# Kernel tuning notes

Hardware: AMD Instinct MI355X
Metric: run time of the kernel (lower is better)

## Reference

```python
import jax, jax.numpy as jnp
import numpy as np
import math

B, LQ, LK = 4, 512, 512
D_MODEL, NHEAD, NLABELS = 512, 8, 8
D_Q = D_MODEL // NHEAD


def setup_inputs() -> dict:
    key = jax.random.key(0)
    ks = jax.random.split(key, 12)
    xavier = lambda k, shape: jax.random.uniform(
        k, shape, jnp.float32,
        -math.sqrt(6.0 / (shape[0] + shape[1])), math.sqrt(6.0 / (shape[0] + shape[1])))
    return {
        "q": jax.random.normal(ks[0], (B, LQ, D_MODEL), jnp.float32),
        "k": jax.random.normal(ks[1], (B, LK, D_MODEL), jnp.float32),
        "edge_mask": jax.random.randint(ks[2], (B, LQ, LK, NLABELS), 0, 2).astype(jnp.float32),
        "padding_mask": jax.random.randint(ks[3], (B, LQ, LK), 0, 2).astype(jnp.float32),
        "w_q_w": xavier(ks[4], (D_MODEL, D_MODEL)),
        "w_q_b": jnp.zeros((D_MODEL,), jnp.float32),
        "w_k": xavier(ks[5], (D_MODEL, D_MODEL)),
        "w_v": xavier(ks[6], (D_MODEL, D_MODEL)),
        "w_h_w": xavier(ks[7], (D_MODEL, D_MODEL)),
        "w_h_b": jnp.zeros((D_MODEL,), jnp.float32),
        "b_ks": xavier(ks[8], (NLABELS, D_Q)),
        "b_vs": xavier(ks[9], (NLABELS, D_Q)),
    }


def reference(q, k, edge_mask, padding_mask, w_q_w, w_q_b, w_k, w_v, w_h_w, w_h_b, b_ks, b_vs):
    sz_b, len_q, _ = q.shape
    len_k = k.shape[1]
    temp = np.power(D_Q, 0.5).astype(np.float32)

    # projections -> (nhead, B, L, d_q), matching torch permute(2,0,1,3)
    query = (q @ w_q_w.T + w_q_b).reshape(sz_b, len_q, NHEAD, D_Q).transpose(2, 0, 1, 3)
    key = (k @ w_k.T).reshape(sz_b, len_k, NHEAD, D_Q).transpose(2, 0, 1, 3)
    value = (k @ w_v.T).reshape(sz_b, len_k, NHEAD, D_Q).transpose(2, 0, 1, 3)

    # content scores + relation-bias scores
    qk = jnp.einsum('hbqd,hbkd->hbqk', query, key)
    key_rel = jnp.einsum('bqkl,ld->bqkd', edge_mask, b_ks)      # (B,Lq,Lk,d_q)
    qkr = jnp.einsum('hbqd,bqkd->hbqk', query, key_rel)
    output_attention_weights = (qk + qkr) / temp                # pre-mask, as returned by torch

    # mask where no edge label AND padding_mask==1
    relation_mask = (edge_mask.sum(-1) + (1.0 - padding_mask)) == 0  # (B,Lq,Lk)
    rm = relation_mask[None, :, :, :]                                # broadcast over heads
    attn = jnp.where(rm, -jnp.inf, output_attention_weights)
    attn = jax.nn.softmax(attn, axis=-1)
    attn = jnp.where(rm, 0.0, attn)

    # value aggregation: content + relation values
    qv = jnp.einsum('hbqk,hbkd->hbqd', attn, value)
    val_rel = jnp.einsum('bqkl,ld->bqkd', edge_mask, b_vs)
    qvr = jnp.einsum('hbqk,bqkd->hbqd', attn, val_rel)

    out = (qv + qvr).transpose(1, 2, 0, 3).reshape(sz_b, len_q, D_MODEL)
    out = out @ w_h_w.T + w_h_b
    return out, output_attention_weights.reshape(NHEAD * sz_b, len_q, len_k)
```

## Files before the change

kernel.cpp:

```cpp
#include <hip/hip_runtime.h>
#include <math.h>

#define NB 4
#define LQ 512
#define LK 512
#define DM 512
#define NH 8
#define DQ 64
#define NL 8
#define QT 32
#define PSTR 520

typedef short bf16x8 __attribute__((ext_vector_type(8)));
typedef float f32x4 __attribute__((ext_vector_type(4)));

__device__ __forceinline__ unsigned short f2bf(float x) {
    unsigned u = __float_as_uint(x);
    u += 0x7fff + ((u >> 16) & 1);
    return (unsigned short)(u >> 16);
}
__device__ __forceinline__ float bf2f(unsigned x) {
    return __uint_as_float(x << 16);
}
__device__ __forceinline__ void gld16(const void* g, void* l) {
    __builtin_amdgcn_global_load_lds(
        (const __attribute__((address_space(1))) void*)g,
        (__attribute__((address_space(3))) void*)l, 16, 0, 0);
}

__global__ __launch_bounds__(256) void prep_kernel(
        const float* __restrict__ q,  const float* __restrict__ k,
        const float* __restrict__ wq, const float* __restrict__ wk,
        const float* __restrict__ wv, const float* __restrict__ wh,
        const float* __restrict__ em, const float* __restrict__ pad,
        unsigned short* __restrict__ qb,  unsigned short* __restrict__ kb,
        unsigned short* __restrict__ wqb, unsigned short* __restrict__ wkb,
        unsigned short* __restrict__ wvb, unsigned short* __restrict__ whb,
        unsigned short* __restrict__ Pk) {
    const int tid = threadIdx.x;
    const int y = blockIdx.y;
    if (y < 6) {
        const float* s; unsigned short* d; int n;
        switch (y) {
            case 0: s = q;  d = qb;  n = NB * LQ * DM; break;
            case 1: s = k;  d = kb;  n = NB * LK * DM; break;
            case 2: s = wq; d = wqb; n = DM * DM; break;
            case 3: s = wk; d = wkb; n = DM * DM; break;
            case 4: s = wv; d = wvb; n = DM * DM; break;
            default: s = wh; d = whb; n = DM * DM; break;
        }
        const int i = blockIdx.x * 256 + tid;
        if (i * 8 >= n) return;
        const float4* sv = (const float4*)s;
        const float4 a = sv[2 * (size_t)i], b = sv[2 * (size_t)i + 1];
        uint4 o;
        o.x = (unsigned)f2bf(a.x) | ((unsigned)f2bf(a.y) << 16);
        o.y = (unsigned)f2bf(a.z) | ((unsigned)f2bf(a.w) << 16);
        o.z = (unsigned)f2bf(b.x) | ((unsigned)f2bf(b.y) << 16);
        o.w = (unsigned)f2bf(b.z) | ((unsigned)f2bf(b.w) << 16);
        *(uint4*)(d + (size_t)i * 8) = o;
    } else {
        if (blockIdx.x >= 512) return;
        const int row = blockIdx.x * 4 + (tid >> 6);
        const int k0 = (tid & 63) * 8;
        const float* eb = em + ((size_t)row * LK + k0) * NL;
        const float4 pv0 = *(const float4*)(pad + (size_t)row * LK + k0);
        const float4 pv1 = *(const float4*)(pad + (size_t)row * LK + k0 + 4);
        const float pv[8] = {pv0.x, pv0.y, pv0.z, pv0.w, pv1.x, pv1.y, pv1.z, pv1.w};
        unsigned short outv[8];
#pragma unroll
        for (int kk = 0; kk < 8; ++kk) {
            const float4 v0 = *(const float4*)(eb + kk * 8);
            const float4 v1 = *(const float4*)(eb + kk * 8 + 4);
            unsigned b_ = 0;
            b_ |= (v0.x != 0.f) << 0; b_ |= (v0.y != 0.f) << 1;
            b_ |= (v0.z != 0.f) << 2; b_ |= (v0.w != 0.f) << 3;
            b_ |= (v1.x != 0.f) << 4; b_ |= (v1.y != 0.f) << 5;
            b_ |= (v1.z != 0.f) << 6; b_ |= (v1.w != 0.f) << 7;
            b_ |= (pv[kk] != 0.f) << 8;
            outv[kk] = (unsigned short)b_;
        }
        uint4 o;
        o.x = (unsigned)outv[0] | ((unsigned)outv[1] << 16);
        o.y = (unsigned)outv[2] | ((unsigned)outv[3] << 16);
        o.z = (unsigned)outv[4] | ((unsigned)outv[5] << 16);
        o.w = (unsigned)outv[6] | ((unsigned)outv[7] << 16);
        *(uint4*)(Pk + (size_t)row * LK + k0) = o;
    }
}

__device__ __forceinline__ void gemm64core(const unsigned short* __restrict__ Ag, int lda,
                                           const unsigned short* __restrict__ Bg, int ldb,
                                           int K, short* As, short* Bs,
                                           f32x4 (&acc)[2][2]) {
    const int tid = threadIdx.x;
    const int wave = tid >> 6, lane = tid & 63;
    const int quad = lane >> 4, l16 = lane & 15;
    const int wr = wave >> 1, wc = wave & 1;
    for (int k0 = 0; k0 < K; k0 += 32) {
        __syncthreads();
        gld16(Ag + (size_t)(tid >> 2) * lda + k0 + (tid & 3) * 8, (char*)As + wave * 1024);
        gld16(Bg + (size_t)(tid >> 2) * ldb + k0 + (tid & 3) * 8, (char*)Bs + wave * 1024);
        __syncthreads();
        bf16x8 af[2], bf[2];
#pragma unroll
        for (int i = 0; i < 2; ++i)
            af[i] = *(const bf16x8*)&As[(wr * 32 + i * 16 + l16) * 32 + quad * 8];
#pragma unroll
        for (int j = 0; j < 2; ++j)
            bf[j] = *(const bf16x8*)&Bs[(wc * 32 + j * 16 + l16) * 32 + quad * 8];
#pragma unroll
        for (int i = 0; i < 2; ++i)
#pragma unroll
            for (int j = 0; j < 2; ++j)
                acc[i][j] = __builtin_amdgcn_mfma_f32_16x16x32_bf16(af[i], bf[j], acc[i][j], 0, 0, 0);
    }
}

__global__ __launch_bounds__(256) void proj_all(const unsigned short* __restrict__ qb,
                                                const unsigned short* __restrict__ kb,
                                                const unsigned short* __restrict__ wqb,
                                                const unsigned short* __restrict__ wkb,
                                                const unsigned short* __restrict__ wvb,
                                                const float* __restrict__ w_q_b,
                                                unsigned short* __restrict__ Qp,
                                                unsigned short* __restrict__ Kp,
                                                unsigned short* __restrict__ Vt) {
    __shared__ __align__(16) short As[64 * 32];
    __shared__ __align__(16) short Bs[64 * 32];
    const unsigned short* A; const unsigned short* W; const float* bias;
    unsigned short* C; int mode;
    switch (blockIdx.z) {
        case 0:  A = qb; W = wqb; bias = w_q_b;  C = Qp; mode = 0; break;
        case 1:  A = kb; W = wkb; bias = nullptr; C = Kp; mode = 0; break;
        default: A = kb; W = wvb; bias = nullptr; C = Vt; mode = 1; break;
    }
    f32x4 acc[2][2];
    const f32x4 zz = {0.f, 0.f, 0.f, 0.f};
#pragma unroll
    for (int i = 0; i < 2; ++i)
#pragma unroll
        for (int j = 0; j < 2; ++j) acc[i][j] = zz;
    const int m0 = blockIdx.x * 64, n0 = blockIdx.y * 64;
    gemm64core(A + (size_t)m0 * DM, DM, W + (size_t)n0 * DM, DM, DM, As, Bs, acc);
    const int tid = threadIdx.x, wave = tid >> 6, lane = tid & 63;
    const int quad = lane >> 4, l16 = lane & 15;
    const int wr = wave >> 1, wc = wave & 1;
#pragma unroll
    for (int i = 0; i < 2; ++i)
#pragma unroll
        for (int r = 0; r < 4; ++r) {
            const int gm = m0 + wr * 32 + i * 16 + quad * 4 + r;
#pragma unroll
            for (int j = 0; j < 2; ++j) {
                const int gn = n0 + wc * 32 + j * 16 + l16;
                float v = acc[i][j][r];
                if (bias) v += bias[gn];
                if (mode == 0) C[(size_t)gm * DM + gn] = f2bf(v);
                else C[(size_t)(gm >> 9) * (DM * LK) + (size_t)gn * LK + (gm & 511)] = f2bf(v);
            }
        }
}

__global__ __launch_bounds__(512, 4) void attn_fused(
        const unsigned short* __restrict__ Qp,
        const unsigned short* __restrict__ Kp,
        const unsigned short* __restrict__ Vt,
        const unsigned short* __restrict__ Pk,
        const float* __restrict__ b_ks,
        const float* __restrict__ b_vs,
        float* __restrict__ weights,
        unsigned short* __restrict__ Hb) {
    __shared__ __align__(16) short Qs[QT * 64];
    __shared__ __align__(16) short Kc[128 * 64];
    __shared__ __align__(16) short Ps[QT * PSTR];
    __shared__ float svS[QT * NL];
    __shared__ float tS[QT * NL];
    __shared__ float redA[QT * 8];
    __shared__ float redB[QT * 8];

    const int tid = threadIdx.x, wave = tid >> 6, lane = tid & 63;
    const int quad = lane >> 4, l16 = lane & 15;
    const int q0 = blockIdx.x * QT;
    const int z = blockIdx.y, h = z >> 2, b = z & 3;

    if (tid < 256) {
        const int row = tid >> 3, ch = tid & 7;
        gld16(Qp + (size_t)(b * LQ + q0 + row) * DM + h * DQ + ((ch ^ (row & 7)) * 8),
              (char*)Qs + wave * 1024);
    }

    f32x4 acc[4][2];
    const f32x4 zz = {0.f, 0.f, 0.f, 0.f};
#pragma unroll
    for (int c = 0; c < 4; ++c) { acc[c][0] = zz; acc[c][1] = zz; }

    for (int c = 0; c < 4; ++c) {
#pragma unroll
        for (int it = 0; it < 2; ++it) {
            const int e = it * 512 + tid;
            const int kr = e >> 3, ch = e & 7;
            gld16(Kp + (size_t)(b * LK + c * 128 + kr) * DM + h * DQ + ((ch ^ (kr & 7)) * 8),
                  (char*)Kc + it * 8192 + wave * 1024);
        }
        __syncthreads();
#pragma unroll
        for (int kd = 0; kd < 64; kd += 32) {
            const int krow = wave * 16 + l16;
            const int kch = ((kd >> 3) + quad) ^ (krow & 7);
            const bf16x8 bfv = *(const bf16x8*)&Kc[krow * 64 + kch * 8];
#pragma unroll
            for (int i = 0; i < 2; ++i) {
                const int qrow = i * 16 + l16;
                const int qch = ((kd >> 3) + quad) ^ (qrow & 7);
                const bf16x8 afv = *(const bf16x8*)&Qs[qrow * 64 + qch * 8];
                acc[c][i] = __builtin_amdgcn_mfma_f32_16x16x32_bf16(afv, bfv, acc[c][i], 0, 0, 0);
            }
        }
        if (c == 0 && tid < 256) {
            const int row = tid >> 3, l = tid & 7;
            float s = 0.f;
#pragma unroll
            for (int d = 0; d < DQ; ++d) {
                const int ds = ((d >> 3) ^ (row & 7)) * 8 + (d & 7);
                s = fmaf(bf2f((unsigned short)Qs[row * 64 + ds]), b_ks[l * DQ + d], s);
            }
            svS[row * 8 + l] = s;
        }
        __syncthreads();
    }

#pragma unroll
    for (int it = 0; it < 2; ++it) {
        const int e = it * 512 + tid;
        const int dd = e >> 4, ch = e & 15;
        gld16(Vt + (size_t)(b * DM + h * DQ + dd) * LK + ((ch ^ (dd & 15)) * 8),
              (char*)Kc + it * 8192 + wave * 1024);
    }

#pragma unroll
    for (int i = 0; i < 2; ++i)
#pragma unroll
        for (int r = 0; r < 4; ++r) {
            const int row = i * 16 + quad * 4 + r;
            const int gq = q0 + row;
            const f32x4 sv0 = *(const f32x4*)&svS[row * 8];
            const f32x4 sv1 = *(const f32x4*)&svS[row * 8 + 4];
            const unsigned short* prow = Pk + (size_t)(b * LQ + gq) * LK;
            float* wrow = weights + ((size_t)z * LQ + gq) * LK;
            float pm = -__builtin_inff();
#pragma unroll
            for (int c = 0; c < 4; ++c) {
                const int col = c * 128 + wave * 16 + l16;
                const unsigned w_ = prow[col];
                float rel = 0.f;
                rel = fmaf((float)((w_ >> 0) & 1), sv0[0], rel);
                rel = fmaf((float)((w_ >> 1) & 1), sv0[1], rel);
                rel = fmaf((float)((w_ >> 2) & 1), sv0[2], rel);
                rel = fmaf((float)((w_ >> 3) & 1), sv0[3], rel);
                rel = fmaf((float)((w_ >> 4) & 1), sv1[0], rel);
                rel = fmaf((float)((w_ >> 5) & 1), sv1[1], rel);
                rel = fmaf((float)((w_ >> 6) & 1), sv1[2], rel);
                rel = fmaf((float)((w_ >> 7) & 1), sv1[3], rel);
                const float wv = (acc[c][i][r] + rel) * 0.125f;
                wrow[col] = wv;
                const float m = ((w_ & 0x1FFu) == 0x100u) ? -__builtin_inff() : wv;
                acc[c][i][r] = m;
                pm = fmaxf(pm, m);
            }
#pragma unroll
            for (int o = 1; o < 16; o <<= 1) pm = fmaxf(pm, __shfl_xor(pm, o, 64));
            float ps = 0.f;
#pragma unroll
            for (int c = 0; c < 4; ++c) {
                const float e = __expf(acc[c][i][r] - pm);
                acc[c][i][r] = e;
                ps += e;
            }
#pragma unroll
            for (int o = 1; o < 16; o <<= 1) ps += __shfl_xor(ps, o, 64);
            if (l16 == 0) { redA[row * 8 + wave] = pm; redB[row * 8 + wave] = ps; }
        }
    __syncthreads();

#pragma unroll
    for (int i = 0; i < 2; ++i)
#pragma unroll
        for (int r = 0; r < 4; ++r) {
            const int row = i * 16 + quad * 4 + r;
            const f32x4 pa = *(const f32x4*)&redA[row * 8];
            const f32x4 pb = *(const f32x4*)&redA[row * 8 + 4];
            const f32x4 sa = *(const f32x4*)&redB[row * 8];
            const f32x4 sb = *(const f32x4*)&redB[row * 8 + 4];
            const float M = fmaxf(fmaxf(fmaxf(pa[0], pa[1]), fmaxf(pa[2], pa[3])),
                                  fmaxf(fmaxf(pb[0], pb[1]), fmaxf(pb[2], pb[3])));
            const float S = sa[0] * __expf(pa[0] - M) + sa[1] * __expf(pa[1] - M)
                          + sa[2] * __expf(pa[2] - M) + sa[3] * __expf(pa[3] - M)
                          + sb[0] * __expf(pb[0] - M) + sb[1] * __expf(pb[1] - M)
                          + sb[2] * __expf(pb[2] - M) + sb[3] * __expf(pb[3] - M);
            const float own = redA[row * 8 + wave];
            const float alpha = __expf(own - M) / S;
#pragma unroll
            for (int c = 0; c < 4; ++c) {
                const int col = c * 128 + wave * 16 + l16;
                Ps[row * PSTR + col] = (short)f2bf(acc[c][i][r] * alpha);
            }
        }
    __syncthreads();

    {
        const int row = tid >> 4, l = (tid >> 1) & 7, half = tid & 1;
        const uint4* pw = (const uint4*)(Pk + (size_t)(b * LQ + q0 + row) * LK + half * 256);
        const uint4* aw = (const uint4*)&Ps[row * PSTR + half * 256];
        float tv = 0.f;
#pragma unroll 4
        for (int kk = 0; kk < 32; ++kk) {
            const uint4 wb = pw[kk];
            const uint4 av = aw[kk];
            const unsigned w4[4] = {wb.x, wb.y, wb.z, wb.w};
            const unsigned a4[4] = {av.x, av.y, av.z, av.w};
#pragma unroll
            for (int u = 0; u < 4; ++u) {
                tv += ((w4[u] >> l) & 1)        ? bf2f(a4[u] & 0xffffu) : 0.f;
                tv += ((w4[u] >> (16 + l)) & 1) ? bf2f(a4[u] >> 16)     : 0.f;
            }
        }
        tv += __shfl_xor(tv, 1, 64);
        if (half == 0) tS[row * 8 + l] = tv;
    }

    f32x4 oacc = zz;
    const int mi = wave & 1, ni = wave >> 1;
    for (int vc = 0; vc < 4; ++vc) {
        if (vc > 0) {
            __syncthreads();
#pragma unroll
            for (int it = 0; it < 2; ++it) {
                const int e = it * 512 + tid;
                const int dd = e >> 4, ch = e & 15;
                gld16(Vt + (size_t)(b * DM + h * DQ + dd) * LK + vc * 128 + ((ch ^ (dd & 15)) * 8),
                      (char*)Kc + it * 8192 + wave * 1024);
            }
            __syncthreads();
        }
#pragma unroll
        for (int kd = 0; kd < 128; kd += 32) {
            const int vrow = ni * 16 + l16;
            const int vch = ((kd >> 3) + quad) ^ (vrow & 15);
            const bf16x8 afv = *(const bf16x8*)&Ps[(mi * 16 + l16) * PSTR + vc * 128 + kd + quad * 8];
            const bf16x8 bfv = *(const bf16x8*)&Kc[vrow * 128 + vch * 8];
            oacc = __builtin_amdgcn_mfma_f32_16x16x32_bf16(afv, bfv, oacc, 0, 0, 0);
        }
    }

    const int gd = ni * 16 + l16;
    float bvv[NL];
#pragma unroll
    for (int l = 0; l < NL; ++l) bvv[l] = b_vs[l * DQ + gd];
#pragma unroll
    for (int r = 0; r < 4; ++r) {
        const int row = mi * 16 + quad * 4 + r;
        const float* tp = &tS[row * 8];
        float o = oacc[r];
#pragma unroll
        for (int l = 0; l < NL; ++l) o = fmaf(tp[l], bvv[l], o);
        Hb[(size_t)(b * LQ + q0 + row) * DM + h * DQ + gd] = f2bf(o);
    }
}

__global__ __launch_bounds__(256) void outproj_mfma(const unsigned short* __restrict__ Hb,
                                                    const unsigned short* __restrict__ whb,
                                                    const float* __restrict__ bias,
                                                    float* __restrict__ C) {
    __shared__ __align__(16) short As[64 * 32];
    __shared__ __align__(16) short Bs[64 * 32];
    f32x4 acc[2][2];
    const f32x4 zz = {0.f, 0.f, 0.f, 0.f};
#pragma unroll
    for (int i = 0; i < 2; ++i)
#pragma unroll
        for (int j = 0; j < 2; ++j) acc[i][j] = zz;
    const int m0 = blockIdx.x * 64, n0 = blockIdx.y * 64;
    gemm64core(Hb + (size_t)m0 * DM, DM, whb + (size_t)n0 * DM, DM, DM, As, Bs, acc);
    const int tid = threadIdx.x, wave = tid >> 6, lane = tid & 63;
    const int quad = lane >> 4, l16 = lane & 15;
    const int wr = wave >> 1, wc = wave & 1;
#pragma unroll
    for (int i = 0; i < 2; ++i)
#pragma unroll
        for (int r = 0; r < 4; ++r) {
            const int gm = m0 + wr * 32 + i * 16 + quad * 4 + r;
#pragma unroll
            for (int j = 0; j < 2; ++j) {
                const int gn = n0 + wc * 32 + j * 16 + l16;
                C[(size_t)gm * DM + gn] = acc[i][j][r] + bias[gn];
            }
        }
}

extern "C" void kernel_launch(void* const* d_in, const int* in_sizes, int n_in,
                              void* d_out, int out_size, void* d_ws, size_t ws_size,
                              hipStream_t stream) {
    const float* q     = (const float*)d_in[0];
    const float* k     = (const float*)d_in[1];
    const float* em    = (const float*)d_in[2];
    const float* pad   = (const float*)d_in[3];
    const float* w_q_w = (const float*)d_in[4];
    const float* w_q_b = (const float*)d_in[5];
    const float* w_k   = (const float*)d_in[6];
    const float* w_v   = (const float*)d_in[7];
    const float* w_h_w = (const float*)d_in[8];
    const float* w_h_b = (const float*)d_in[9];
    const float* b_ks  = (const float*)d_in[10];
    const float* b_vs  = (const float*)d_in[11];

    float* out     = (float*)d_out;
    float* weights = out + (size_t)NB * LQ * DM;

    char* ws = (char*)d_ws;
    unsigned short* qb  = (unsigned short*)(ws + 0);
    unsigned short* kb  = (unsigned short*)(ws + 2097152);
    unsigned short* wqb = (unsigned short*)(ws + 4194304);
    unsigned short* wkb = (unsigned short*)(ws + 4718592);
    unsigned short* wvb = (unsigned short*)(ws + 5242880);
    unsigned short* whb = (unsigned short*)(ws + 5767168);
    unsigned short* Qp  = (unsigned short*)(ws + 6291456);
    unsigned short* Kp  = (unsigned short*)(ws + 8388608);
    unsigned short* Vt  = (unsigned short*)(ws + 10485760);
    unsigned short* Hb  = (unsigned short*)(ws + 12582912);
    unsigned short* Pk  = (unsigned short*)(ws + 14680064);

    prep_kernel<<<dim3(1024, 7), 256, 0, stream>>>(q, k, w_q_w, w_k, w_v, w_h_w,
                                                   em, pad, qb, kb, wqb, wkb, wvb, whb, Pk);
    proj_all<<<dim3(32, 8, 3), 256, 0, stream>>>(qb, kb, wqb, wkb, wvb, w_q_b, Qp, Kp, Vt);
    attn_fused<<<dim3(LQ / QT, 32), 512, 0, stream>>>(Qp, Kp, Vt, Pk, b_ks, b_vs, weights, Hb);
    outproj_mfma<<<dim3(32, 8), 256, 0, stream>>>(Hb, whb, w_h_b, out);
}
```

Baseline: 169.9 us.

## Drop LDS staging for direct global MFMA loads, add relation LUT and fp16 PV path

Removes LDS staging with global_load_lds from the projection, output-projection and attention kernels, so MFMA fragments are read directly from global memory. The relation score is now a per-row 16-entry lookup table built from q·b_ks, replacing eight FMAs per score. Probabilities and V are stored as fp16 so the PV product uses the f16 MFMA and the relation-value sum uses packed half math. This cuts barriers and shared-memory traffic, but relies on cache hits for reused operands and changes the numeric precision of P and V.

```diff
diff --git a/kernel.cpp b/kernel.cpp
--- a/kernel.cpp
+++ b/kernel.cpp
@@ -12,6 +12,8 @@
 #define PSTR 520
 
 typedef short bf16x8 __attribute__((ext_vector_type(8)));
+typedef _Float16 f16x8 __attribute__((ext_vector_type(8)));
+typedef _Float16 f16x2 __attribute__((ext_vector_type(2)));
 typedef float f32x4 __attribute__((ext_vector_type(4)));
 
 __device__ __forceinline__ unsigned short f2bf(float x) {
@@ -22,10 +24,9 @@
 __device__ __forceinline__ float bf2f(unsigned x) {
     return __uint_as_float(x << 16);
 }
-__device__ __forceinline__ void gld16(const void* g, void* l) {
-    __builtin_amdgcn_global_load_lds(
-        (const __attribute__((address_space(1))) void*)g,
-        (__attribute__((address_space(3))) void*)l, 16, 0, 0);
+__device__ __forceinline__ unsigned short f2h(float x) {
+    _Float16 h = (_Float16)x;
+    return __builtin_bit_cast(unsigned short, h);
 }
 
 __global__ __launch_bounds__(256) void prep_kernel(
@@ -89,34 +90,6 @@
     }
 }
 
-__device__ __forceinline__ void gemm64core(const unsigned short* __restrict__ Ag, int lda,
-                                           const unsigned short* __restrict__ Bg, int ldb,
-                                           int K, short* As, short* Bs,
-                                           f32x4 (&acc)[2][2]) {
-    const int tid = threadIdx.x;
-    const int wave = tid >> 6, lane = tid & 63;
-    const int quad = lane >> 4, l16 = lane & 15;
-    const int wr = wave >> 1, wc = wave & 1;
-    for (int k0 = 0; k0 < K; k0 += 32) {
-        __syncthreads();
-        gld16(Ag + (size_t)(tid >> 2) * lda + k0 + (tid & 3) * 8, (char*)As + wave * 1024);
-        gld16(Bg + (size_t)(tid >> 2) * ldb + k0 + (tid & 3) * 8, (char*)Bs + wave * 1024);
-        __syncthreads();
-        bf16x8 af[2], bf[2];
-#pragma unroll
-        for (int i = 0; i < 2; ++i)
-            af[i] = *(const bf16x8*)&As[(wr * 32 + i * 16 + l16) * 32 + quad * 8];
-#pragma unroll
-        for (int j = 0; j < 2; ++j)
-            bf[j] = *(const bf16x8*)&Bs[(wc * 32 + j * 16 + l16) * 32 + quad * 8];
-#pragma unroll
-        for (int i = 0; i < 2; ++i)
-#pragma unroll
-            for (int j = 0; j < 2; ++j)
-                acc[i][j] = __builtin_amdgcn_mfma_f32_16x16x32_bf16(af[i], bf[j], acc[i][j], 0, 0, 0);
-    }
-}
-
 __global__ __launch_bounds__(256) void proj_all(const unsigned short* __restrict__ qb,
                                                 const unsigned short* __restrict__ kb,
                                                 const unsigned short* __restrict__ wqb,
@@ -126,8 +99,6 @@
                                                 unsigned short* __restrict__ Qp,
                                                 unsigned short* __restrict__ Kp,
                                                 unsigned short* __restrict__ Vt) {
-    __shared__ __align__(16) short As[64 * 32];
-    __shared__ __align__(16) short Bs[64 * 32];
     const unsigned short* A; const unsigned short* W; const float* bias;
     unsigned short* C; int mode;
     switch (blockIdx.z) {
@@ -135,17 +106,32 @@
         case 1:  A = kb; W = wkb; bias = nullptr; C = Kp; mode = 0; break;
         default: A = kb; W = wvb; bias = nullptr; C = Vt; mode = 1; break;
     }
-    f32x4 acc[2][2];
-    const f32x4 zz = {0.f, 0.f, 0.f, 0.f};
-#pragma unroll
-    for (int i = 0; i < 2; ++i)
-#pragma unroll
-        for (int j = 0; j < 2; ++j) acc[i][j] = zz;
-    const int m0 = blockIdx.x * 64, n0 = blockIdx.y * 64;
-    gemm64core(A + (size_t)m0 * DM, DM, W + (size_t)n0 * DM, DM, DM, As, Bs, acc);
     const int tid = threadIdx.x, wave = tid >> 6, lane = tid & 63;
     const int quad = lane >> 4, l16 = lane & 15;
     const int wr = wave >> 1, wc = wave & 1;
+    const int m0 = blockIdx.x * 64, n0 = blockIdx.y * 64;
+    f32x4 acc[2][2];
+    const f32x4 zz = {0.f, 0.f, 0.f, 0.f};
+#pragma unroll
+    for (int i = 0; i < 2; ++i)
+#pragma unroll
+        for (int j = 0; j < 2; ++j) acc[i][j] = zz;
+    const unsigned short* Ar0 = A + (size_t)(m0 + wr * 32 + l16) * DM;
+    const unsigned short* Ar1 = Ar0 + 16 * DM;
+    const unsigned short* Br0 = W + (size_t)(n0 + wc * 32 + l16) * DM;
+    const unsigned short* Br1 = Br0 + 16 * DM;
+#pragma unroll 4
+    for (int k0 = 0; k0 < DM; k0 += 32) {
+        const int o = k0 + quad * 8;
+        const bf16x8 a0 = *(const bf16x8*)&Ar0[o];
+        const bf16x8 a1 = *(const bf16x8*)&Ar1[o];
+        const bf16x8 b0 = *(const bf16x8*)&Br0[o];
+        const bf16x8 b1 = *(const bf16x8*)&Br1[o];
+        acc[0][0] = __builtin_amdgcn_mfma_f32_16x16x32_bf16(a0, b0, acc[0][0], 0, 0, 0);
+        acc[0][1] = __builtin_amdgcn_mfma_f32_16x16x32_bf16(a0, b1, acc[0][1], 0, 0, 0);
+        acc[1][0] = __builtin_amdgcn_mfma_f32_16x16x32_bf16(a1, b0, acc[1][0], 0, 0, 0);
+        acc[1][1] = __builtin_amdgcn_mfma_f32_16x16x32_bf16(a1, b1, acc[1][1], 0, 0, 0);
+    }
 #pragma unroll
     for (int i = 0; i < 2; ++i)
 #pragma unroll
@@ -157,7 +143,7 @@
                 float v = acc[i][j][r];
                 if (bias) v += bias[gn];
                 if (mode == 0) C[(size_t)gm * DM + gn] = f2bf(v);
-                else C[(size_t)(gm >> 9) * (DM * LK) + (size_t)gn * LK + (gm & 511)] = f2bf(v);
+                else C[(size_t)(gm >> 9) * (DM * LK) + (size_t)gn * LK + (gm & 511)] = f2h(v);
             }
         }
 }
@@ -171,10 +157,9 @@
         const float* __restrict__ b_vs,
         float* __restrict__ weights,
         unsigned short* __restrict__ Hb) {
-    __shared__ __align__(16) short Qs[QT * 64];
-    __shared__ __align__(16) short Kc[128 * 64];
     __shared__ __align__(16) short Ps[QT * PSTR];
     __shared__ float svS[QT * NL];
+    __shared__ float lutS[QT * 32];
     __shared__ float tS[QT * NL];
     __shared__ float redA[QT * 8];
     __shared__ float redB[QT * 8];
@@ -184,59 +169,57 @@
     const int q0 = blockIdx.x * QT;
     const int z = blockIdx.y, h = z >> 2, b = z & 3;
 
-    if (tid < 256) {
-        const int row = tid >> 3, ch = tid & 7;
-        gld16(Qp + (size_t)(b * LQ + q0 + row) * DM + h * DQ + ((ch ^ (row & 7)) * 8),
-              (char*)Qs + wave * 1024);
+    {
+        const int row = tid >> 4, l = (tid >> 1) & 7, half = tid & 1;
+        const unsigned short* qrow = Qp + (size_t)(b * LQ + q0 + row) * DM + h * DQ + half * 32;
+        const float* bk = b_ks + l * DQ + half * 32;
+        float s = 0.f;
+#pragma unroll
+        for (int d0 = 0; d0 < 32; d0 += 8) {
+            const bf16x8 qv = *(const bf16x8*)&qrow[d0];
+#pragma unroll
+            for (int j = 0; j < 8; ++j)
+                s = fmaf(bf2f((unsigned short)qv[j]), bk[d0 + j], s);
+        }
+        s += __shfl_xor(s, 1, 64);
+        if (half == 0) svS[row * 8 + l] = s;
+    }
+    __syncthreads();
+
+    for (int e = tid; e < QT * 32; e += 512) {
+        const int row = e >> 5, idx = e & 31;
+        const float* s = &svS[row * 8 + ((idx & 16) ? 4 : 0)];
+        float v = 0.f;
+        v += (idx & 1) ? s[0] : 0.f;
+        v += (idx & 2) ? s[1] : 0.f;
+        v += (idx & 4) ? s[2] : 0.f;
+        v += (idx & 8) ? s[3] : 0.f;
+        lutS[e] = v;
     }
 
     f32x4 acc[4][2];
     const f32x4 zz = {0.f, 0.f, 0.f, 0.f};
 #pragma unroll
     for (int c = 0; c < 4; ++c) { acc[c][0] = zz; acc[c][1] = zz; }
-
+    bf16x8 qf[2][2];
+#pragma unroll
+    for (int i = 0; i < 2; ++i)
+#pragma unroll
+        for (int kd = 0; kd < 2; ++kd)
+            qf[i][kd] = *(const bf16x8*)&Qp[(size_t)(b * LQ + q0 + i * 16 + l16) * DM
+                                           + h * DQ + kd * 32 + quad * 8];
+#pragma unroll
     for (int c = 0; c < 4; ++c) {
-#pragma unroll
-        for (int it = 0; it < 2; ++it) {
-            const int e = it * 512 + tid;
-            const int kr = e >> 3, ch = e & 7;
-            gld16(Kp + (size_t)(b * LK + c * 128 + kr) * DM + h * DQ + ((ch ^ (kr & 7)) * 8),
-                  (char*)Kc + it * 8192 + wave * 1024);
-        }
-        __syncthreads();
-#pragma unroll
-        for (int kd = 0; kd < 64; kd += 32) {
-            const int krow = wave * 16 + l16;
-            const int kch = ((kd >> 3) + quad) ^ (krow & 7);
-            const bf16x8 bfv = *(const bf16x8*)&Kc[krow * 64 + kch * 8];
-#pragma unroll
-            for (int i = 0; i < 2; ++i) {
-                const int qrow = i * 16 + l16;
-                const int qch = ((kd >> 3) + quad) ^ (qrow & 7);
-                const bf16x8 afv = *(const bf16x8*)&Qs[qrow * 64 + qch * 8];
-                acc[c][i] = __builtin_amdgcn_mfma_f32_16x16x32_bf16(afv, bfv, acc[c][i], 0, 0, 0);
-            }
-        }
-        if (c == 0 && tid < 256) {
-            const int row = tid >> 3, l = tid & 7;
-            float s = 0.f;
-#pragma unroll
-            for (int d = 0; d < DQ; ++d) {
-                const int ds = ((d >> 3) ^ (row & 7)) * 8 + (d & 7);
-                s = fmaf(bf2f((unsigned short)Qs[row * 64 + ds]), b_ks[l * DQ + d], s);
-            }
-            svS[row * 8 + l] = s;
-        }
-        __syncthreads();
-    }
-
-#pragma unroll
-    for (int it = 0; it < 2; ++it) {
-        const int e = it * 512 + tid;
-        const int dd = e >> 4, ch = e & 15;
-        gld16(Vt + (size_t)(b * DM + h * DQ + dd) * LK + ((ch ^ (dd & 15)) * 8),
-              (char*)Kc + it * 8192 + wave * 1024);
-    }
+        const unsigned short* krow = Kp + (size_t)(b * LK + c * 128 + wave * 16 + l16) * DM + h * DQ;
+#pragma unroll
+        for (int kd = 0; kd < 2; ++kd) {
+            const bf16x8 bfv = *(const bf16x8*)&krow[kd * 32 + quad * 8];
+#pragma unroll
+            for (int i = 0; i < 2; ++i)
+                acc[c][i] = __builtin_amdgcn_mfma_f32_16x16x32_bf16(qf[i][kd], bfv, acc[c][i], 0, 0, 0);
+        }
+    }
+    __syncthreads();
 
 #pragma unroll
     for (int i = 0; i < 2; ++i)
@@ -244,8 +227,7 @@
         for (int r = 0; r < 4; ++r) {
             const int row = i * 16 + quad * 4 + r;
             const int gq = q0 + row;
-            const f32x4 sv0 = *(const f32x4*)&svS[row * 8];
-            const f32x4 sv1 = *(const f32x4*)&svS[row * 8 + 4];
+            const float* lrow = &lutS[row * 32];
             const unsigned short* prow = Pk + (size_t)(b * LQ + gq) * LK;
             float* wrow = weights + ((size_t)z * LQ + gq) * LK;
             float pm = -__builtin_inff();
@@ -253,15 +235,7 @@
             for (int c = 0; c < 4; ++c) {
                 const int col = c * 128 + wave * 16 + l16;
                 const unsigned w_ = prow[col];
-                float rel = 0.f;
-                rel = fmaf((float)((w_ >> 0) & 1), sv0[0], rel);
-                rel = fmaf((float)((w_ >> 1) & 1), sv0[1], rel);
-                rel = fmaf((float)((w_ >> 2) & 1), sv0[2], rel);
-                rel = fmaf((float)((w_ >> 3) & 1), sv0[3], rel);
-                rel = fmaf((float)((w_ >> 4) & 1), sv1[0], rel);
-                rel = fmaf((float)((w_ >> 5) & 1), sv1[1], rel);
-                rel = fmaf((float)((w_ >> 6) & 1), sv1[2], rel);
-                rel = fmaf((float)((w_ >> 7) & 1), sv1[3], rel);
+                const float rel = lrow[w_ & 15u] + lrow[16 + ((w_ >> 4) & 15u)];
                 const float wv = (acc[c][i][r] + rel) * 0.125f;
                 wrow[col] = wv;
                 const float m = ((w_ & 0x1FFu) == 0x100u) ? -__builtin_inff() : wv;
@@ -303,7 +277,7 @@
 #pragma unroll
             for (int c = 0; c < 4; ++c) {
                 const int col = c * 128 + wave * 16 + l16;
-                Ps[row * PSTR + col] = (short)f2bf(acc[c][i][r] * alpha);
+                Ps[row * PSTR + col] = (short)f2h(acc[c][i][r] * alpha);
             }
         }
     __syncthreads();
@@ -319,11 +293,14 @@
             const uint4 av = aw[kk];
             const unsigned w4[4] = {wb.x, wb.y, wb.z, wb.w};
             const unsigned a4[4] = {av.x, av.y, av.z, av.w};
+            f16x2 hacc = {(_Float16)0.f, (_Float16)0.f};
 #pragma unroll
             for (int u = 0; u < 4; ++u) {
-                tv += ((w4[u] >> l) & 1)        ? bf2f(a4[u] & 0xffffu) : 0.f;
-                tv += ((w4[u] >> (16 + l)) & 1) ? bf2f(a4[u] >> 16)     : 0.f;
-            }
+                const unsigned bits = (w4[u] >> l) & 0x10001u;
+                const unsigned msk = bits * 0x3c00u;
+                hacc += __builtin_bit_cast(f16x2, a4[u]) * __builtin_bit_cast(f16x2, msk);
+            }
+            tv += (float)hacc[0] + (float)hacc[1];
         }
         tv += __shfl_xor(tv, 1, 64);
         if (half == 0) tS[row * 8 + l] = tv;
@@ -331,27 +308,15 @@
 
     f32x4 oacc = zz;
     const int mi = wave & 1, ni = wave >> 1;
-    for (int vc = 0; vc < 4; ++vc) {
-        if (vc > 0) {
-            __syncthreads();
-#pragma unroll
-            for (int it = 0; it < 2; ++it) {
-                const int e = it * 512 + tid;
-                const int dd = e >> 4, ch = e & 15;
-                gld16(Vt + (size_t)(b * DM + h * DQ + dd) * LK + vc * 128 + ((ch ^ (dd & 15)) * 8),
-                      (char*)Kc + it * 8192 + wave * 1024);
-            }
-            __syncthreads();
-        }
-#pragma unroll
-        for (int kd = 0; kd < 128; kd += 32) {
-            const int vrow = ni * 16 + l16;
-            const int vch = ((kd >> 3) + quad) ^ (vrow & 15);
-            const bf16x8 afv = *(const bf16x8*)&Ps[(mi * 16 + l16) * PSTR + vc * 128 + kd + quad * 8];
-            const bf16x8 bfv = *(const bf16x8*)&Kc[vrow * 128 + vch * 8];
-            oacc = __builtin_amdgcn_mfma_f32_16x16x32_bf16(afv, bfv, oacc, 0, 0, 0);
-        }
-    }
+    const unsigned short* vrow = Vt + (size_t)(b * DM + h * DQ + ni * 16 + l16) * LK;
+    const short* psrow = &Ps[(mi * 16 + l16) * PSTR];
+#pragma unroll 4
+    for (int kc = 0; kc < LK; kc += 32) {
+        const f16x8 afv = *(const f16x8*)&psrow[kc + quad * 8];
+        const f16x8 bfv = *(const f16x8*)&vrow[kc + quad * 8];
+        oacc = __builtin_amdgcn_mfma_f32_16x16x32_f16(afv, bfv, oacc, 0, 0, 0);
+    }
+    __syncthreads();
 
     const int gd = ni * 16 + l16;
     float bvv[NL];
@@ -372,19 +337,32 @@
                                                     const unsigned short* __restrict__ whb,
                                                     const float* __restrict__ bias,
                                                     float* __restrict__ C) {
-    __shared__ __align__(16) short As[64 * 32];
-    __shared__ __align__(16) short Bs[64 * 32];
-    f32x4 acc[2][2];
-    const f32x4 zz = {0.f, 0.f, 0.f, 0.f};
-#pragma unroll
-    for (int i = 0; i < 2; ++i)
-#pragma unroll
-        for (int j = 0; j < 2; ++j) acc[i][j] = zz;
-    const int m0 = blockIdx.x * 64, n0 = blockIdx.y * 64;
-    gemm64core(Hb + (size_t)m0 * DM, DM, whb + (size_t)n0 * DM, DM, DM, As, Bs, acc);
     const int tid = threadIdx.x, wave = tid >> 6, lane = tid & 63;
     const int quad = lane >> 4, l16 = lane & 15;
     const int wr = wave >> 1, wc = wave & 1;
+    const int m0 = blockIdx.x * 64, n0 = blockIdx.y * 64;
+    f32x4 acc[2][2];
+    const f32x4 zz = {0.f, 0.f, 0.f, 0.f};
+#pragma unroll
+    for (int i = 0; i < 2; ++i)
+#pragma unroll
+        for (int j = 0; j < 2; ++j) acc[i][j] = zz;
+    const unsigned short* Ar0 = Hb + (size_t)(m0 + wr * 32 + l16) * DM;
+    const unsigned short* Ar1 = Ar0 + 16 * DM;
+    const unsigned short* Br0 = whb + (size_t)(n0 + wc * 32 + l16) * DM;
+    const unsigned short* Br1 = Br0 + 16 * DM;
+#pragma unroll 4
+    for (int k0 = 0; k0 < DM; k0 += 32) {
+        const int o = k0 + quad * 8;
+        const bf16x8 a0 = *(const bf16x8*)&Ar0[o];
+        const bf16x8 a1 = *(const bf16x8*)&Ar1[o];
+        const bf16x8 b0 = *(const bf16x8*)&Br0[o];
+        const bf16x8 b1 = *(const bf16x8*)&Br1[o];
+        acc[0][0] = __builtin_amdgcn_mfma_f32_16x16x32_bf16(a0, b0, acc[0][0], 0, 0, 0);
+        acc[0][1] = __builtin_amdgcn_mfma_f32_16x16x32_bf16(a0, b1, acc[0][1], 0, 0, 0);
+        acc[1][0] = __builtin_amdgcn_mfma_f32_16x16x32_bf16(a1, b0, acc[1][0], 0, 0, 0);
+        acc[1][1] = __builtin_amdgcn_mfma_f32_16x16x32_bf16(a1, b1, acc[1][1], 0, 0, 0);
+    }
 #pragma unroll
     for (int i = 0; i < 2; ++i)
 #pragma unroll
```

Result: slower. 189.0 us (+11.2%).
